# Performance work log

Hardware: AMD Instinct MI355X
Metric: run time of the kernel (lower is better)

## Reference

```python
import jax, jax.numpy as jnp
import numpy as np

B = 32768
MAXD = 60               # max raw feature dim (user)
DIMS = [60, 51, 43]     # user, event, space
H = 256                 # HIDDEN_DIM
E = 256                 # EMBED_DIM
NH = 4                  # num heads
HD = H // NH            # head dim = 64
SCALE = float(np.sqrt(HD))
EPS = 1e-5


def setup_inputs() -> dict:
    key = jax.random.key(0)
    ks = iter(jax.random.split(key, 64))
    def rn(shape, scale=0.05):
        return jax.random.normal(next(ks), shape, dtype=jnp.float32) * scale
    inp = {}
    inp["anchor_feats"] = jax.random.normal(next(ks), (B, MAXD), dtype=jnp.float32)
    inp["item_feats"] = jax.random.normal(next(ks), (B, MAXD), dtype=jnp.float32)
    inp["anchor_type_ids"] = jax.random.randint(next(ks), (B,), 0, 3, dtype=jnp.int32)
    inp["item_type_ids"] = jax.random.randint(next(ks), (B,), 0, 3, dtype=jnp.int32)
    # per-type encoder MLPs; W1 zero-padded beyond each type's input dim (matches torch slicing x[:, :dim])
    W1 = rn((3, MAXD, H))
    row_mask = np.zeros((3, MAXD, 1), dtype=np.float32)
    for t, d in enumerate(DIMS):
        row_mask[t, :d, 0] = 1.0
    inp["enc_W1"] = W1 * jnp.asarray(row_mask)
    inp["enc_b1"] = rn((3, H)); inp["enc_g1"] = jnp.ones((3, H)); inp["enc_be1"] = jnp.zeros((3, H))
    inp["enc_W2"] = rn((3, H, H))
    inp["enc_b2"] = rn((3, H)); inp["enc_g2"] = jnp.ones((3, H)); inp["enc_be2"] = jnp.zeros((3, H))
    # two stacked HGT layers; 9 edge types (src*3+dst), 3 node types
    inp["hgt_Wk"] = rn((2, 9, H, H)); inp["hgt_Wq"] = rn((2, 9, H, H)); inp["hgt_Wv"] = rn((2, 9, H, H))
    inp["hgt_Wout"] = rn((2, 3, H, H))
    inp["hgt_g"] = jnp.ones((2, 3, H)); inp["hgt_b"] = jnp.zeros((2, 3, H))
    inp["out_W"] = rn((H, E)); inp["out_b"] = rn((E,))
    inp["out_g"] = jnp.ones((E,)); inp["out_be"] = jnp.zeros((E,))
    return inp


def _ln(x, g, b):
    m = x.mean(-1, keepdims=True)
    v = ((x - m) ** 2).mean(-1, keepdims=True)
    return (x - m) / jnp.sqrt(v + EPS) * g + b


def _encode(feats, tids, W1, b1, g1, be1, W2, b2, g2, be2):
    # per-type 2-layer MLP (Linear->LN->ReLU x2, dropout=eval noop), masked select
    h = jnp.zeros((feats.shape[0], H), feats.dtype)
    for t in range(3):
        z = jax.nn.relu(_ln(feats @ W1[t] + b1[t], g1[t], be1[t]))
        z = jax.nn.relu(_ln(z @ W2[t] + b2[t], g2[t], be2[t]))
        h = jnp.where((tids == t)[:, None], z, h)
    return h


def _hgt_apply(Wk, Wq, Wv, Wout, g, b, e, dt, src_h, dst_h):
    # single-dim dot-product attention per head, sigmoid gate
    Bn = src_h.shape[0]
    k = (src_h @ Wk[e]).reshape(Bn, NH, HD)
    q = (dst_h @ Wq[e]).reshape(Bn, NH, HD)
    v = (src_h @ Wv[e]).reshape(Bn, NH, HD)
    attn = jax.nn.sigmoid((q * k).sum(-1, keepdims=True) / SCALE)
    msg = (attn * v).reshape(Bn, H)
    return _ln(dst_h + msg @ Wout[dt], g[dt], b[dt])


def _hgt_hop(Wk, Wq, Wv, Wout, g, b, ha, hi, atid, itid):
    # torch code: ha_out from clone of ha, hi updated per disjoint (atype,itype) mask,
    # both updates read ORIGINAL ha/hi for each masked element
    ha_new, hi_new = ha, hi
    for a in range(3):
        for i in range(3):
            mask = ((atid == a) & (itid == i))[:, None]
            ua = _hgt_apply(Wk, Wq, Wv, Wout, g, b, i * 3 + a, a, hi, ha)  # item -> anchor
            ui = _hgt_apply(Wk, Wq, Wv, Wout, g, b, a * 3 + i, i, ha, hi)  # anchor -> item
            ha_new = jnp.where(mask, ua, ha_new)
            hi_new = jnp.where(mask, ui, hi_new)
    return ha_new, hi_new


def _l2norm(x):
    return x / jnp.maximum(jnp.linalg.norm(x, axis=-1, keepdims=True), 1e-12)


def reference(anchor_feats, item_feats, anchor_type_ids, item_type_ids,
              enc_W1, enc_b1, enc_g1, enc_be1, enc_W2, enc_b2, enc_g2, enc_be2,
              hgt_Wk, hgt_Wq, hgt_Wv, hgt_Wout, hgt_g, hgt_b,
              out_W, out_b, out_g, out_be):
    ha = _encode(anchor_feats, anchor_type_ids, enc_W1, enc_b1, enc_g1, enc_be1, enc_W2, enc_b2, enc_g2, enc_be2)
    hi = _encode(item_feats, item_type_ids, enc_W1, enc_b1, enc_g1, enc_be1, enc_W2, enc_b2, enc_g2, enc_be2)
    for L in range(2):
        ha, hi = _hgt_hop(hgt_Wk[L], hgt_Wq[L], hgt_Wv[L], hgt_Wout[L], hgt_g[L], hgt_b[L],
                          ha, hi, anchor_type_ids, item_type_ids)
    anchor_emb = _l2norm(_ln(ha @ out_W + out_b, out_g, out_be))
    item_emb = _l2norm(_ln(hi @ out_W + out_b, out_g, out_be))
    return anchor_emb, item_emb
```

## Files before the change

### kernel.cpp

```cpp
#include <hip/hip_runtime.h>
#include <math.h>

#define BN   32768
#define MAXD 60
#define HDIM 256
#define TR   16
#define LDX  264

typedef __attribute__((ext_vector_type(4))) float f32x4;
typedef __attribute__((ext_vector_type(8))) short bf16x8;

#define MFMA(a, b, c) __builtin_amdgcn_mfma_f32_16x16x32_bf16(a, b, c, 0, 0, 0)

__device__ __forceinline__ unsigned short f2bf(float f) {
  union { float f; unsigned u; } v; v.f = f;
  unsigned r = v.u + 0x7FFF + ((v.u >> 16) & 1);
  return (unsigned short)(r >> 16);
}

template <int LDXE>
__device__ __forceinline__ bf16x8 ldsAx(const unsigned short* buf, int rf,
                                        int ks, int lane) {
  const int row = rf * 16 + (lane & 15);
  const int ko = ks * 32 + ((lane >> 4) << 3);
  return *(const bf16x8*)(buf + row * LDXE + ko);
}

template <int KS>
__device__ __forceinline__ bf16x8 fragB(const unsigned short* __restrict__ W,
                                        int cfw, int ks, int lane) {
  return *(const bf16x8*)(W + ((size_t)(cfw * KS + ks) << 9) + (lane << 3));
}

__device__ __forceinline__ float red16(float p) {
  p += __shfl_xor(p, 1); p += __shfl_xor(p, 2);
  p += __shfl_xor(p, 4); p += __shfl_xor(p, 8);
  return p;
}

__device__ __forceinline__ void cross_ln(float* redS, float* redQ,
                                         const float sums[2][4],
                                         const float sumq[2][4], int lane,
                                         int wid, float mo[2][4],
                                         float ro[2][4]) {
  __syncthreads();
  if ((lane & 15) == 0) {
    #pragma unroll
    for (int rf = 0; rf < 2; ++rf)
      #pragma unroll
      for (int rr = 0; rr < 4; ++rr) {
        const int row = rf * 16 + ((lane >> 4) << 2) + rr;
        redS[row * 4 + wid] = sums[rf][rr];
        redQ[row * 4 + wid] = sumq[rf][rr];
      }
  }
  __syncthreads();
  #pragma unroll
  for (int rf = 0; rf < 2; ++rf)
    #pragma unroll
    for (int rr = 0; rr < 4; ++rr) {
      const int row = rf * 16 + ((lane >> 4) << 2) + rr;
      float s = redS[row * 4] + redS[row * 4 + 1] + redS[row * 4 + 2] + redS[row * 4 + 3];
      float z = redQ[row * 4] + redQ[row * 4 + 1] + redQ[row * 4 + 2] + redQ[row * 4 + 3];
      float m = s * (1.0f / HDIM);
      mo[rf][rr] = m;
      ro[rf][rr] = rsqrtf(z * (1.0f / HDIM) - m * m + 1e-5f);
    }
}


__device__ __forceinline__ void row_reduce(float* red, const float acc[TR],
                                           float m[TR], float rs[TR], int j) {
  const int lane = j & 63, wv = j >> 6;
  __syncthreads();
  #pragma unroll
  for (int r = 0; r < TR; ++r) {
    float s = acc[r], q = acc[r] * acc[r];
    #pragma unroll
    for (int o = 32; o; o >>= 1) { s += __shfl_xor(s, o); q += __shfl_xor(q, o); }
    if (lane == 0) { red[r * 8 + wv * 2] = s; red[r * 8 + wv * 2 + 1] = q; }
  }
  __syncthreads();
  #pragma unroll
  for (int r = 0; r < TR; ++r) {
    float s = red[r * 8 + 0] + red[r * 8 + 2] + red[r * 8 + 4] + red[r * 8 + 6];
    float q = red[r * 8 + 1] + red[r * 8 + 3] + red[r * 8 + 5] + red[r * 8 + 7];
    float mean = s * (1.0f / HDIM);
    float var  = q * (1.0f / HDIM) - mean * mean;
    m[r]  = mean;
    rs[r] = rsqrtf(var + 1e-5f);
  }
}

template <int KD, int ST>
__device__ __forceinline__ void matvec_l(const float* __restrict__ W,
                                         const float* zz, float acc[TR], int j) {
  #pragma unroll 2
  for (int k = 0; k < KD; k += 4) {
    const float w0 = W[(k + 0) * HDIM + j];
    const float w1 = W[(k + 1) * HDIM + j];
    const float w2 = W[(k + 2) * HDIM + j];
    const float w3 = W[(k + 3) * HDIM + j];
    #pragma unroll
    for (int r = 0; r < TR; ++r) {
      const float4 x = *(const float4*)(zz + r * ST + k);
      acc[r] = fmaf(x.w, w3, fmaf(x.z, w2, fmaf(x.y, w1, fmaf(x.x, w0, acc[r]))));
    }
  }
}


__global__ __launch_bounds__(256) void bucket_kernel(
    const int* __restrict__ atid, const int* __restrict__ itid,
    int* cnts, int* idxA, int* idxI, int* idxC) {
  __shared__ int lcnt[15], lbase[15];
  const int tid = threadIdx.x;
  const int r = blockIdx.x * 256 + tid;
  if (tid < 15) lcnt[tid] = 0;
  __syncthreads();
  const int a = atid[r], i = itid[r];
  const int c = a * 3 + i;
  const int la = atomicAdd(&lcnt[a], 1);
  const int li = atomicAdd(&lcnt[3 + i], 1);
  const int lc = atomicAdd(&lcnt[6 + c], 1);
  __syncthreads();
  if (tid < 15) lbase[tid] = atomicAdd(&cnts[tid], lcnt[tid]);
  __syncthreads();
  idxA[a * BN + lbase[a] + la] = r;
  idxI[i * BN + lbase[3 + i] + li] = r;
  idxC[c * BN + lbase[6 + c] + lc] = r;
}


__global__ __launch_bounds__(256) void wpack_kernel(
    const float* __restrict__ src, unsigned short* __restrict__ dst,
    int nmat, int KS, int srcK) {
  const int per = KS * 8192;
  const int idx = blockIdx.x * 256 + threadIdx.x;
  const int m = idx / per;
  if (m >= nmat) return;
  const int r = idx % per;
  const int e = r & 7;
  const int lane = (r >> 3) & 63;
  const int t = r >> 9;
  const int ks = t % KS;
  const int cfw = t / KS;
  const int n = ((cfw >> 2) << 6) + ((cfw & 3) << 4) + (lane & 15);
  const int k = (ks << 5) + ((lane >> 4) << 3) + e;
  const float v = (k < srcK) ? src[(size_t)m * srcK * 256 + (size_t)k * 256 + n] : 0.0f;
  dst[idx] = f2bf(v);
}


struct EncSmem {
  unsigned short x1[32 * 72];
  unsigned short z[32 * LDX];
  float redS[32 * 4];
  float redQ[32 * 4];
  int rowsL[32];
};

__global__ __launch_bounds__(256) void enc_mfma_kernel(
    const float* __restrict__ af, const float* __restrict__ itf,
    const int* __restrict__ idxA, const int* __restrict__ idxI,
    const int* __restrict__ cnts,
    const unsigned short* __restrict__ pW1, const unsigned short* __restrict__ pW2,
    const float* __restrict__ b1, const float* __restrict__ g1,
    const float* __restrict__ be1, const float* __restrict__ b2,
    const float* __restrict__ g2, const float* __restrict__ be2,
    float* __restrict__ ha, float* __restrict__ hi) {
  const int t = blockIdx.y, ent = blockIdx.z;
  const int cnt = cnts[ent * 3 + t];
  const int base = blockIdx.x * 32;
  if (base >= cnt) return;
  const float* feats = ent ? itf : af;
  const int* idx = (ent ? idxI : idxA) + t * BN;
  float* hout = ent ? hi : ha;
  __shared__ EncSmem sm;
  const int tid = threadIdx.x, lane = tid & 63, wid = tid >> 6;

  if (tid < 32) {
    int rr = base + tid; if (rr > cnt - 1) rr = cnt - 1;
    sm.rowsL[tid] = idx[rr];
  }
  __syncthreads();
  {
    const int c2 = (tid & 31) * 2, rh = tid >> 5;
    #pragma unroll
    for (int p = 0; p < 4; ++p) {
      const int r = p * 8 + rh;
      unsigned val = 0;
      if (c2 < MAXD) {
        const float2 v = *(const float2*)(feats + (size_t)sm.rowsL[r] * MAXD + c2);
        val = (unsigned)f2bf(v.x) | ((unsigned)f2bf(v.y) << 16);
      }
      *(unsigned*)(sm.x1 + r * 72 + c2) = val;
    }
  }
  int mg[8];
  #pragma unroll
  for (int rf = 0; rf < 2; ++rf)
    #pragma unroll
    for (int rr = 0; rr < 4; ++rr)
      mg[rf * 4 + rr] = sm.rowsL[rf * 16 + ((lane >> 4) << 2) + rr];
  __syncthreads();

  f32x4 acc[2][4] = {};
  #pragma unroll
  for (int ks = 0; ks < 2; ++ks) {
    bf16x8 a0 = ldsAx<72>(sm.x1, 0, ks, lane);
    bf16x8 a1 = ldsAx<72>(sm.x1, 1, ks, lane);
    #pragma unroll
    for (int cf = 0; cf < 4; ++cf) {
      bf16x8 w = fragB<2>(pW1 + (size_t)t * 16384, (wid << 2) + cf, ks, lane);
      acc[0][cf] = MFMA(a0, w, acc[0][cf]);
      acc[1][cf] = MFMA(a1, w, acc[1][cf]);
    }
  }
  float cb[4], cg[4], cbe[4];
  #pragma unroll
  for (int cf = 0; cf < 4; ++cf) {
    const int col = (wid << 6) + (cf << 4) + (lane & 15);
    cb[cf] = b1[t * HDIM + col]; cg[cf] = g1[t * HDIM + col]; cbe[cf] = be1[t * HDIM + col];
  }
  float sums[2][4] = {}, sumq[2][4] = {};
  #pragma unroll
  for (int rf = 0; rf < 2; ++rf)
    #pragma unroll
    for (int cf = 0; cf < 4; ++cf)
      #pragma unroll
      for (int rr = 0; rr < 4; ++rr) {
        float x = acc[rf][cf][rr] + cb[cf];
        acc[rf][cf][rr] = x;
        sums[rf][rr] += x; sumq[rf][rr] += x * x;
      }
  #pragma unroll
  for (int rf = 0; rf < 2; ++rf)
    #pragma unroll
    for (int rr = 0; rr < 4; ++rr) { sums[rf][rr] = red16(sums[rf][rr]); sumq[rf][rr] = red16(sumq[rf][rr]); }
  float m[2][4], rs[2][4];
  cross_ln(sm.redS, sm.redQ, sums, sumq, lane, wid, m, rs);
  #pragma unroll
  for (int rf = 0; rf < 2; ++rf)
    #pragma unroll
    for (int cf = 0; cf < 4; ++cf) {
      const int col = (wid << 6) + (cf << 4) + (lane & 15);
      #pragma unroll
      for (int rr = 0; rr < 4; ++rr) {
        const int row = rf * 16 + ((lane >> 4) << 2) + rr;
        float zz = fmaxf((acc[rf][cf][rr] - m[rf][rr]) * rs[rf][rr] * cg[cf] + cbe[cf], 0.0f);
        sm.z[row * LDX + col] = f2bf(zz);
      }
    }
  __syncthreads();

  #pragma unroll
  for (int rf = 0; rf < 2; ++rf)
    #pragma unroll
    for (int cf = 0; cf < 4; ++cf) acc[rf][cf] = (f32x4){0.f, 0.f, 0.f, 0.f};
  #pragma unroll 2
  for (int ks = 0; ks < 8; ++ks) {
    bf16x8 a0 = ldsAx<LDX>(sm.z, 0, ks, lane);
    bf16x8 a1 = ldsAx<LDX>(sm.z, 1, ks, lane);
    #pragma unroll
    for (int cf = 0; cf < 4; ++cf) {
      bf16x8 w = fragB<8>(pW2 + (size_t)t * 65536, (wid << 2) + cf, ks, lane);
      acc[0][cf] = MFMA(a0, w, acc[0][cf]);
      acc[1][cf] = MFMA(a1, w, acc[1][cf]);
    }
  }
  #pragma unroll
  for (int cf = 0; cf < 4; ++cf) {
    const int col = (wid << 6) + (cf << 4) + (lane & 15);
    cb[cf] = b2[t * HDIM + col]; cg[cf] = g2[t * HDIM + col]; cbe[cf] = be2[t * HDIM + col];
  }
  float sums2[2][4] = {}, sumq2[2][4] = {};
  #pragma unroll
  for (int rf = 0; rf < 2; ++rf)
    #pragma unroll
    for (int cf = 0; cf < 4; ++cf)
      #pragma unroll
      for (int rr = 0; rr < 4; ++rr) {
        float x = acc[rf][cf][rr] + cb[cf];
        acc[rf][cf][rr] = x;
        sums2[rf][rr] += x; sumq2[rf][rr] += x * x;
      }
  #pragma unroll
  for (int rf = 0; rf < 2; ++rf)
    #pragma unroll
    for (int rr = 0; rr < 4; ++rr) { sums2[rf][rr] = red16(sums2[rf][rr]); sumq2[rf][rr] = red16(sumq2[rf][rr]); }
  cross_ln(sm.redS, sm.redQ, sums2, sumq2, lane, wid, m, rs);
  #pragma unroll
  for (int rf = 0; rf < 2; ++rf)
    #pragma unroll
    for (int cf = 0; cf < 4; ++cf) {
      const int col = (wid << 6) + (cf << 4) + (lane & 15);
      #pragma unroll
      for (int rr = 0; rr < 4; ++rr)
        hout[(size_t)mg[rf * 4 + rr] * HDIM + col] =
            fmaxf((acc[rf][cf][rr] - m[rf][rr]) * rs[rf][rr] * cg[cf] + cbe[cf], 0.0f);
    }
}


struct HopSmem {
  unsigned short xa[32 * LDX];
  unsigned short xi[32 * LDX];
  unsigned short msg[32 * LDX];
  float redS[32 * 4];
  float redQ[32 * 4];
  int rowsL[32];
};

__device__ __forceinline__ void hop_dir(
    const unsigned short* __restrict__ bq, const unsigned short* __restrict__ bk,
    const unsigned short* __restrict__ bv, const unsigned short* __restrict__ bo,
    const float* __restrict__ gg, const float* __restrict__ bb,
    const unsigned short* xdst, const unsigned short* xsrc,
    const float* __restrict__ hdst_g, float* __restrict__ hout_g,
    HopSmem& sm, const int mg[8], int lane, int wid) {
  f32x4 q[2][4] = {}; f32x4 kk[2][4] = {};
  #pragma unroll 2
  for (int ks = 0; ks < 8; ++ks) {
    bf16x8 ad0 = ldsAx<LDX>(xdst, 0, ks, lane), ad1 = ldsAx<LDX>(xdst, 1, ks, lane);
    bf16x8 as0 = ldsAx<LDX>(xsrc, 0, ks, lane), as1 = ldsAx<LDX>(xsrc, 1, ks, lane);
    #pragma unroll
    for (int cf = 0; cf < 4; ++cf) {
      bf16x8 wq = fragB<8>(bq, (wid << 2) + cf, ks, lane);
      bf16x8 wk = fragB<8>(bk, (wid << 2) + cf, ks, lane);
      q[0][cf]  = MFMA(ad0, wq, q[0][cf]);
      q[1][cf]  = MFMA(ad1, wq, q[1][cf]);
      kk[0][cf] = MFMA(as0, wk, kk[0][cf]);
      kk[1][cf] = MFMA(as1, wk, kk[1][cf]);
    }
  }
  float at[2][4];
  #pragma unroll
  for (int rf = 0; rf < 2; ++rf)
    #pragma unroll
    for (int rr = 0; rr < 4; ++rr) {
      float p = q[rf][0][rr] * kk[rf][0][rr] + q[rf][1][rr] * kk[rf][1][rr]
              + q[rf][2][rr] * kk[rf][2][rr] + q[rf][3][rr] * kk[rf][3][rr];
      p = red16(p);
      at[rf][rr] = 1.0f / (1.0f + __expf(-p * 0.125f));
    }
  f32x4 vv[2][4] = {};
  #pragma unroll 2
  for (int ks = 0; ks < 8; ++ks) {
    bf16x8 as0 = ldsAx<LDX>(xsrc, 0, ks, lane), as1 = ldsAx<LDX>(xsrc, 1, ks, lane);
    #pragma unroll
    for (int cf = 0; cf < 4; ++cf) {
      bf16x8 wv = fragB<8>(bv, (wid << 2) + cf, ks, lane);
      vv[0][cf] = MFMA(as0, wv, vv[0][cf]);
      vv[1][cf] = MFMA(as1, wv, vv[1][cf]);
    }
  }
  __syncthreads();
  #pragma unroll
  for (int rf = 0; rf < 2; ++rf)
    #pragma unroll
    for (int cf = 0; cf < 4; ++cf) {
      const int col = (wid << 6) + (cf << 4) + (lane & 15);
      #pragma unroll
      for (int rr = 0; rr < 4; ++rr) {
        const int row = rf * 16 + ((lane >> 4) << 2) + rr;
        sm.msg[row * LDX + col] = f2bf(vv[rf][cf][rr] * at[rf][rr]);
      }
    }
  __syncthreads();
  f32x4 oo[2][4] = {};
  #pragma unroll 2
  for (int ks = 0; ks < 8; ++ks) {
    bf16x8 am0 = ldsAx<LDX>(sm.msg, 0, ks, lane), am1 = ldsAx<LDX>(sm.msg, 1, ks, lane);
    #pragma unroll
    for (int cf = 0; cf < 4; ++cf) {
      bf16x8 wo = fragB<8>(bo, (wid << 2) + cf, ks, lane);
      oo[0][cf] = MFMA(am0, wo, oo[0][cf]);
      oo[1][cf] = MFMA(am1, wo, oo[1][cf]);
    }
  }
  float sums[2][4] = {}, sumq[2][4] = {};
  #pragma unroll
  for (int rf = 0; rf < 2; ++rf)
    #pragma unroll
    for (int cf = 0; cf < 4; ++cf) {
      const int col = (wid << 6) + (cf << 4) + (lane & 15);
      #pragma unroll
      for (int rr = 0; rr < 4; ++rr) {
        float x = hdst_g[(size_t)mg[rf * 4 + rr] * HDIM + col] + oo[rf][cf][rr];
        oo[rf][cf][rr] = x;
        sums[rf][rr] += x;
        sumq[rf][rr] += x * x;
      }
    }
  #pragma unroll
  for (int rf = 0; rf < 2; ++rf)
    #pragma unroll
    for (int rr = 0; rr < 4; ++rr) { sums[rf][rr] = red16(sums[rf][rr]); sumq[rf][rr] = red16(sumq[rf][rr]); }
  float m[2][4], rs[2][4];
  cross_ln(sm.redS, sm.redQ, sums, sumq, lane, wid, m, rs);
  float g4[4], b4[4];
  #pragma unroll
  for (int cf = 0; cf < 4; ++cf) {
    const int col = (wid << 6) + (cf << 4) + (lane & 15);
    g4[cf] = gg[col]; b4[cf] = bb[col];
  }
  #pragma unroll
  for (int rf = 0; rf < 2; ++rf)
    #pragma unroll
    for (int rr = 0; rr < 4; ++rr) {
      #pragma unroll
      for (int cf = 0; cf < 4; ++cf) {
        const int col = (wid << 6) + (cf << 4) + (lane & 15);
        hout_g[(size_t)mg[rf * 4 + rr] * HDIM + col] =
            (oo[rf][cf][rr] - m[rf][rr]) * rs[rf][rr] * g4[cf] + b4[cf];
      }
    }
}

__global__ __launch_bounds__(256) void hop_mfma_kernel(
    const unsigned short* __restrict__ bWk, const unsigned short* __restrict__ bWq,
    const unsigned short* __restrict__ bWv, const unsigned short* __restrict__ bWo,
    const float* __restrict__ g, const float* __restrict__ b,
    const int* __restrict__ idxC, const int* __restrict__ cnts,
    float* __restrict__ ha, float* __restrict__ hi) {
  const int c = blockIdx.y, a = c / 3, i = c % 3;
  const int cnt = cnts[6 + c];
  const int base = blockIdx.x * 32;
  if (base >= cnt) return;
  __shared__ HopSmem sm;
  const int tid = threadIdx.x;
  const int lane = tid & 63, wid = tid >> 6;

  if (tid < 32) {
    int rr = base + tid; if (rr > cnt - 1) rr = cnt - 1;
    sm.rowsL[tid] = idxC[c * BN + rr];
  }
  __syncthreads();
  const int cp = (tid & 127) * 2, rh = tid >> 7;
  #pragma unroll 4
  for (int r0 = 0; r0 < 32; r0 += 2) {
    const int r = r0 + rh;
    const size_t gb = (size_t)sm.rowsL[r] * HDIM + cp;
    float2 va = *(const float2*)(ha + gb);
    float2 vi = *(const float2*)(hi + gb);
    *(unsigned*)(sm.xa + r * LDX + cp) =
        (unsigned)f2bf(va.x) | ((unsigned)f2bf(va.y) << 16);
    *(unsigned*)(sm.xi + r * LDX + cp) =
        (unsigned)f2bf(vi.x) | ((unsigned)f2bf(vi.y) << 16);
  }
  int mg[8];
  #pragma unroll
  for (int rf = 0; rf < 2; ++rf)
    #pragma unroll
    for (int rr = 0; rr < 4; ++rr)
      mg[rf * 4 + rr] = sm.rowsL[rf * 16 + ((lane >> 4) << 2) + rr];
  __syncthreads();

  const size_t MS = (size_t)HDIM * HDIM;
  const int e1 = i * 3 + a;
  const int e2 = a * 3 + i;
  hop_dir(bWq + e1 * MS, bWk + e1 * MS, bWv + e1 * MS, bWo + a * MS,
          g + a * HDIM, b + a * HDIM, sm.xa, sm.xi, ha, ha, sm, mg, lane, wid);
  hop_dir(bWq + e2 * MS, bWk + e2 * MS, bWv + e2 * MS, bWo + i * MS,
          g + i * HDIM, b + i * HDIM, sm.xi, sm.xa, hi, hi, sm, mg, lane, wid);
}


struct OutSmem {
  unsigned short x[32 * LDX];
  float redS[32 * 4];
  float redQ[32 * 4];
};

__global__ __launch_bounds__(256) void out_mfma_kernel(
    const unsigned short* __restrict__ pW, const float* __restrict__ bb,
    const float* __restrict__ g, const float* __restrict__ be,
    float* __restrict__ out) {
  const int ent = blockIdx.y;
  const int base = blockIdx.x * 32;
  float* hsrc = out + (size_t)ent * BN * HDIM;
  __shared__ OutSmem sm;
  const int tid = threadIdx.x, lane = tid & 63, wid = tid >> 6;
  const int cp = (tid & 127) * 2, rh = tid >> 7;
  #pragma unroll 4
  for (int r0 = 0; r0 < 32; r0 += 2) {
    const int r = r0 + rh;
    const float2 v = *(const float2*)(hsrc + (size_t)(base + r) * HDIM + cp);
    *(unsigned*)(sm.x + r * LDX + cp) =
        (unsigned)f2bf(v.x) | ((unsigned)f2bf(v.y) << 16);
  }
  __syncthreads();
  f32x4 acc[2][4] = {};
  #pragma unroll 2
  for (int ks = 0; ks < 8; ++ks) {
    bf16x8 a0 = ldsAx<LDX>(sm.x, 0, ks, lane);
    bf16x8 a1 = ldsAx<LDX>(sm.x, 1, ks, lane);
    #pragma unroll
    for (int cf = 0; cf < 4; ++cf) {
      bf16x8 w = fragB<8>(pW, (wid << 2) + cf, ks, lane);
      acc[0][cf] = MFMA(a0, w, acc[0][cf]);
      acc[1][cf] = MFMA(a1, w, acc[1][cf]);
    }
  }
  float cb[4], cg[4], cbe[4];
  #pragma unroll
  for (int cf = 0; cf < 4; ++cf) {
    const int col = (wid << 6) + (cf << 4) + (lane & 15);
    cb[cf] = bb[col]; cg[cf] = g[col]; cbe[cf] = be[col];
  }
  float sums[2][4] = {}, sumq[2][4] = {};
  #pragma unroll
  for (int rf = 0; rf < 2; ++rf)
    #pragma unroll
    for (int cf = 0; cf < 4; ++cf)
      #pragma unroll
      for (int rr = 0; rr < 4; ++rr) {
        float x = acc[rf][cf][rr] + cb[cf];
        acc[rf][cf][rr] = x;
        sums[rf][rr] += x; sumq[rf][rr] += x * x;
      }
  #pragma unroll
  for (int rf = 0; rf < 2; ++rf)
    #pragma unroll
    for (int rr = 0; rr < 4; ++rr) { sums[rf][rr] = red16(sums[rf][rr]); sumq[rf][rr] = red16(sumq[rf][rr]); }
  float m[2][4], rs[2][4];
  cross_ln(sm.redS, sm.redQ, sums, sumq, lane, wid, m, rs);
  float s2[2][4] = {};
  #pragma unroll
  for (int rf = 0; rf < 2; ++rf)
    #pragma unroll
    for (int cf = 0; cf < 4; ++cf)
      #pragma unroll
      for (int rr = 0; rr < 4; ++rr) {
        float y = (acc[rf][cf][rr] - m[rf][rr]) * rs[rf][rr] * cg[cf] + cbe[cf];
        acc[rf][cf][rr] = y;
        s2[rf][rr] += y * y;
      }
  #pragma unroll
  for (int rf = 0; rf < 2; ++rf)
    #pragma unroll
    for (int rr = 0; rr < 4; ++rr) s2[rf][rr] = red16(s2[rf][rr]);
  __syncthreads();
  if ((lane & 15) == 0) {
    #pragma unroll
    for (int rf = 0; rf < 2; ++rf)
      #pragma unroll
      for (int rr = 0; rr < 4; ++rr) {
        const int row = rf * 16 + ((lane >> 4) << 2) + rr;
        sm.redS[row * 4 + wid] = s2[rf][rr];
      }
  }
  __syncthreads();
  #pragma unroll
  for (int rf = 0; rf < 2; ++rf)
    #pragma unroll
    for (int rr = 0; rr < 4; ++rr) {
      const int row = rf * 16 + ((lane >> 4) << 2) + rr;
      float ss = sm.redS[row * 4] + sm.redS[row * 4 + 1] +
                 sm.redS[row * 4 + 2] + sm.redS[row * 4 + 3];
      float inv = 1.0f / fmaxf(sqrtf(ss), 1e-12f);
      #pragma unroll
      for (int cf = 0; cf < 4; ++cf) {
        const int col = (wid << 6) + (cf << 4) + (lane & 15);
        hsrc[(size_t)(base + row) * HDIM + col] = acc[rf][cf][rr] * inv;
      }
    }
}


__global__ __launch_bounds__(256) void enc_kernel(
    const float* __restrict__ af, const float* __restrict__ itf,
    const int* __restrict__ idxA, const int* __restrict__ idxI,
    const int* __restrict__ cnts,
    const float* __restrict__ W1, const float* __restrict__ b1,
    const float* __restrict__ g1, const float* __restrict__ be1,
    const float* __restrict__ W2, const float* __restrict__ b2,
    const float* __restrict__ g2, const float* __restrict__ be2,
    float* __restrict__ ha, float* __restrict__ hi) {
  const int t = blockIdx.y, ent = blockIdx.z;
  const int cnt = cnts[ent * 3 + t];
  const int base = blockIdx.x * TR;
  if (base >= cnt) return;
  const int nr = (cnt - base < TR) ? (cnt - base) : TR;
  const int j = threadIdx.x;
  const float* feats = ent ? itf : af;
  const int* idx = (ent ? idxI : idxA) + t * BN;
  float* hout = ent ? hi : ha;
  __shared__ __align__(16) float xl[TR * 64];
  __shared__ __align__(16) float z[TR * HDIM];
  __shared__ float red[TR * 8];
  int rows[TR];
  #pragma unroll
  for (int r = 0; r < TR; ++r) {
    int rr = base + r; if (rr > cnt - 1) rr = cnt - 1;
    rows[r] = idx[rr];
  }
  if (j < 64) {
    #pragma unroll
    for (int r = 0; r < TR; ++r)
      xl[r * 64 + j] = (j < MAXD) ? feats[(size_t)rows[r] * MAXD + j] : 0.0f;
  }
  __syncthreads();
  float acc[TR];
  const float bj = b1[t * HDIM + j];
  #pragma unroll
  for (int r = 0; r < TR; ++r) acc[r] = bj;
  matvec_l<MAXD, 64>(W1 + (size_t)t * MAXD * HDIM, xl, acc, j);
  float m[TR], rs[TR];
  row_reduce(red, acc, m, rs, j);
  const float g1j = g1[t * HDIM + j], be1j = be1[t * HDIM + j];
  #pragma unroll
  for (int r = 0; r < TR; ++r)
    z[r * HDIM + j] = fmaxf((acc[r] - m[r]) * rs[r] * g1j + be1j, 0.0f);
  __syncthreads();
  const float b2j = b2[t * HDIM + j];
  #pragma unroll
  for (int r = 0; r < TR; ++r) acc[r] = b2j;
  matvec_l<HDIM, HDIM>(W2 + (size_t)t * HDIM * HDIM, z, acc, j);
  row_reduce(red, acc, m, rs, j);
  const float g2j = g2[t * HDIM + j], be2j = be2[t * HDIM + j];
  #pragma unroll
  for (int r = 0; r < TR; ++r)
    if (r < nr)
      hout[(size_t)rows[r] * HDIM + j] =
          fmaxf((acc[r] - m[r]) * rs[r] * g2j + be2j, 0.0f);
}

__device__ __forceinline__ void hgt_dir_f32(
    const float* __restrict__ Wq, const float* __restrict__ Wk,
    const float* __restrict__ Wv, const float* __restrict__ Wo,
    const float* __restrict__ gg, const float* __restrict__ bb,
    const float* dstl, const float* srcl, float* msg, float* red, int j,
    float res[TR]) {
  float q[TR], kk[TR];
  #pragma unroll
  for (int r = 0; r < TR; ++r) { q[r] = 0.0f; kk[r] = 0.0f; }
  matvec_l<HDIM, HDIM>(Wq, dstl, q, j);
  matvec_l<HDIM, HDIM>(Wk, srcl, kk, j);
  float attn[TR];
  #pragma unroll
  for (int r = 0; r < TR; ++r) {
    float p = q[r] * kk[r];
    #pragma unroll
    for (int o = 32; o; o >>= 1) p += __shfl_xor(p, o);
    attn[r] = 1.0f / (1.0f + expf(-p * 0.125f));
  }
  #pragma unroll
  for (int r = 0; r < TR; ++r) q[r] = 0.0f;
  matvec_l<HDIM, HDIM>(Wv, srcl, q, j);
  __syncthreads();
  #pragma unroll
  for (int r = 0; r < TR; ++r) msg[r * HDIM + j] = attn[r] * q[r];
  __syncthreads();
  float o[TR];
  #pragma unroll
  for (int r = 0; r < TR; ++r) o[r] = 0.0f;
  matvec_l<HDIM, HDIM>(Wo, msg, o, j);
  float u[TR], m[TR], rs[TR];
  #pragma unroll
  for (int r = 0; r < TR; ++r) u[r] = dstl[r * HDIM + j] + o[r];
  row_reduce(red, u, m, rs, j);
  const float gj = gg[j], bj = bb[j];
  #pragma unroll
  for (int r = 0; r < TR; ++r) res[r] = (u[r] - m[r]) * rs[r] * gj + bj;
}

__global__ __launch_bounds__(256) void hop_kernel(
    const float* __restrict__ Wk, const float* __restrict__ Wq,
    const float* __restrict__ Wv, const float* __restrict__ Wout,
    const float* __restrict__ g, const float* __restrict__ b,
    const int* __restrict__ idxC, const int* __restrict__ cnts,
    float* __restrict__ ha, float* __restrict__ hi) {
  const int c = blockIdx.y, a = c / 3, i = c % 3;
  const int cnt = cnts[6 + c];
  const int base = blockIdx.x * TR;
  if (base >= cnt) return;
  const int nr = (cnt - base < TR) ? (cnt - base) : TR;
  const int j = threadIdx.x;
  __shared__ __align__(16) float xa[TR * HDIM];
  __shared__ __align__(16) float xi[TR * HDIM];
  __shared__ __align__(16) float msg[TR * HDIM];
  __shared__ float red[TR * 8];
  int rows[TR];
  #pragma unroll
  for (int r = 0; r < TR; ++r) {
    int rr = base + r; if (rr > cnt - 1) rr = cnt - 1;
    rows[r] = idxC[c * BN + rr];
  }
  #pragma unroll
  for (int r = 0; r < TR; ++r) {
    xa[r * HDIM + j] = ha[(size_t)rows[r] * HDIM + j];
    xi[r * HDIM + j] = hi[(size_t)rows[r] * HDIM + j];
  }
  __syncthreads();
  const int e1 = i * 3 + a, e2 = a * 3 + i;
  float res1[TR], res2[TR];
  hgt_dir_f32(Wq + (size_t)e1 * HDIM * HDIM, Wk + (size_t)e1 * HDIM * HDIM,
              Wv + (size_t)e1 * HDIM * HDIM, Wout + (size_t)a * HDIM * HDIM,
              g + a * HDIM, b + a * HDIM, xa, xi, msg, red, j, res1);
  hgt_dir_f32(Wq + (size_t)e2 * HDIM * HDIM, Wk + (size_t)e2 * HDIM * HDIM,
              Wv + (size_t)e2 * HDIM * HDIM, Wout + (size_t)i * HDIM * HDIM,
              g + i * HDIM, b + i * HDIM, xi, xa, msg, red, j, res2);
  #pragma unroll
  for (int r = 0; r < TR; ++r)
    if (r < nr) {
      ha[(size_t)rows[r] * HDIM + j] = res1[r];
      hi[(size_t)rows[r] * HDIM + j] = res2[r];
    }
}

__global__ __launch_bounds__(256) void out_kernel(
    const float* __restrict__ W, const float* __restrict__ bb,
    const float* __restrict__ g, const float* __restrict__ be,
    float* __restrict__ out) {
  const int ent = blockIdx.y;
  const int base = blockIdx.x * TR;
  const int j = threadIdx.x;
  float* hsrc = out + (size_t)ent * BN * HDIM;
  __shared__ __align__(16) float xl[TR * HDIM];
  __shared__ float red[TR * 8];
  #pragma unroll
  for (int r = 0; r < TR; ++r)
    xl[r * HDIM + j] = hsrc[(size_t)(base + r) * HDIM + j];
  __syncthreads();
  float acc[TR];
  const float bj = bb[j];
  #pragma unroll
  for (int r = 0; r < TR; ++r) acc[r] = bj;
  matvec_l<HDIM, HDIM>(W, xl, acc, j);
  float m[TR], rs[TR];
  row_reduce(red, acc, m, rs, j);
  const float gj = g[j], bej = be[j];
  float y[TR];
  #pragma unroll
  for (int r = 0; r < TR; ++r) y[r] = (acc[r] - m[r]) * rs[r] * gj + bej;
  const int lane = j & 63, wv = j >> 6;
  __syncthreads();
  #pragma unroll
  for (int r = 0; r < TR; ++r) {
    float p = y[r] * y[r];
    #pragma unroll
    for (int o = 32; o; o >>= 1) p += __shfl_xor(p, o);
    if (lane == 0) red[r * 4 + wv] = p;
  }
  __syncthreads();
  #pragma unroll
  for (int r = 0; r < TR; ++r) {
    float ss = red[r * 4] + red[r * 4 + 1] + red[r * 4 + 2] + red[r * 4 + 3];
    float inv = 1.0f / fmaxf(sqrtf(ss), 1e-12f);
    hsrc[(size_t)(base + r) * HDIM + j] = y[r] * inv;
  }
}


extern "C" void kernel_launch(void* const* d_in, const int* in_sizes, int n_in,
                              void* d_out, int out_size, void* d_ws,
                              size_t ws_size, hipStream_t stream) {
  const float* af   = (const float*)d_in[0];
  const float* itf  = (const float*)d_in[1];
  const int*   atid = (const int*)d_in[2];
  const int*   itid = (const int*)d_in[3];
  const float* eW1  = (const float*)d_in[4];
  const float* eb1  = (const float*)d_in[5];
  const float* eg1  = (const float*)d_in[6];
  const float* ebe1 = (const float*)d_in[7];
  const float* eW2  = (const float*)d_in[8];
  const float* eb2  = (const float*)d_in[9];
  const float* eg2  = (const float*)d_in[10];
  const float* ebe2 = (const float*)d_in[11];
  const float* hWk  = (const float*)d_in[12];
  const float* hWq  = (const float*)d_in[13];
  const float* hWv  = (const float*)d_in[14];
  const float* hWo  = (const float*)d_in[15];
  const float* hg   = (const float*)d_in[16];
  const float* hb   = (const float*)d_in[17];
  const float* oW   = (const float*)d_in[18];
  const float* ob   = (const float*)d_in[19];
  const float* og   = (const float*)d_in[20];
  const float* obe  = (const float*)d_in[21];

  float* out = (float*)d_out;
  float* ha = out;
  float* hi = out + (size_t)BN * HDIM;

  int* cnts = (int*)d_ws;
  int* idxA = cnts + 16;
  int* idxI = idxA + 3 * BN;
  int* idxC = idxI + 3 * BN;
  unsigned short* pW1 = (unsigned short*)(idxC + 9 * BN);
  unsigned short* pW2 = pW1 + 3 * 16384;
  unsigned short* pWk = pW2 + 3 * 65536;
  unsigned short* pWq = pWk + 18 * 65536;
  unsigned short* pWv = pWq + 18 * 65536;
  unsigned short* pWo = pWv + 18 * 65536;
  unsigned short* pOW = pWo + 6 * 65536;
  const size_t ws_need = (size_t)(16 + 15 * BN) * 4 +
                         ((size_t)3 * 16384 + (size_t)64 * 65536) * 2;
  const bool use_mfma = ws_size >= ws_need;

  hipMemsetAsync(cnts, 0, 16 * sizeof(int), stream);
  bucket_kernel<<<BN / 256, 256, 0, stream>>>(atid, itid, cnts, idxA, idxI, idxC);

  if (use_mfma) {
    wpack_kernel<<<3 * 16384 / 256, 256, 0, stream>>>(eW1, pW1, 3, 2, 60);
    wpack_kernel<<<3 * 65536 / 256, 256, 0, stream>>>(eW2, pW2, 3, 8, 256);
    wpack_kernel<<<18 * 65536 / 256, 256, 0, stream>>>(hWk, pWk, 18, 8, 256);
    wpack_kernel<<<18 * 65536 / 256, 256, 0, stream>>>(hWq, pWq, 18, 8, 256);
    wpack_kernel<<<18 * 65536 / 256, 256, 0, stream>>>(hWv, pWv, 18, 8, 256);
    wpack_kernel<<<6 * 65536 / 256, 256, 0, stream>>>(hWo, pWo, 6, 8, 256);
    wpack_kernel<<<65536 / 256, 256, 0, stream>>>(oW, pOW, 1, 8, 256);

    enc_mfma_kernel<<<dim3(BN / 32, 3, 2), 256, 0, stream>>>(
        af, itf, idxA, idxI, cnts, pW1, pW2,
        eb1, eg1, ebe1, eb2, eg2, ebe2, ha, hi);
    for (int L = 0; L < 2; ++L) {
      hop_mfma_kernel<<<dim3(BN / 32, 9), 256, 0, stream>>>(
          pWk + (size_t)L * 9 * 65536, pWq + (size_t)L * 9 * 65536,
          pWv + (size_t)L * 9 * 65536, pWo + (size_t)L * 3 * 65536,
          hg + L * 3 * HDIM, hb + L * 3 * HDIM, idxC, cnts, ha, hi);
    }
    out_mfma_kernel<<<dim3(BN / 32, 2), 256, 0, stream>>>(pOW, ob, og, obe, out);
  } else {
    enc_kernel<<<dim3((BN + TR - 1) / TR, 3, 2), 256, 0, stream>>>(
        af, itf, idxA, idxI, cnts, eW1, eb1, eg1, ebe1, eW2, eb2, eg2, ebe2,
        ha, hi);
    for (int L = 0; L < 2; ++L) {
      hop_kernel<<<dim3((BN + TR - 1) / TR, 9), 256, 0, stream>>>(
          hWk + (size_t)L * 9 * HDIM * HDIM, hWq + (size_t)L * 9 * HDIM * HDIM,
          hWv + (size_t)L * 9 * HDIM * HDIM, hWo + (size_t)L * 3 * HDIM * HDIM,
          hg + L * 3 * HDIM, hb + L * 3 * HDIM, idxC, cnts, ha, hi);
    }
    out_kernel<<<dim3(BN / TR, 2), 256, 0, stream>>>(oW, ob, og, obe, out);
  }
}
```

Before: 324.2 us.

## Fuse encoder, both HGT hops and output projection into one per-pair kernel

Replaces the separate encoder, two hop, and output kernels with one fused kernel. Each block handles 32 rows of one (anchor type, item type) pair and keeps the anchor and item hidden states in registers and LDS across all stages. This removes the fp32 global round trips of ha/hi between stages and several kernel launches. In exchange, the encoder work is grouped by pair bucket and blocks carry more register state. The LDS row stride also changes from 264 to 260.

```diff
diff --git a/kernel.cpp b/kernel.cpp
--- a/kernel.cpp
+++ b/kernel.cpp
@@ -5,7 +5,7 @@
 #define MAXD 60
 #define HDIM 256
 #define TR   16
-#define LDX  264
+#define LDX  260
 
 typedef __attribute__((ext_vector_type(4))) float f32x4;
 typedef __attribute__((ext_vector_type(8))) short bf16x8;
@@ -37,6 +37,15 @@
   p += __shfl_xor(p, 4); p += __shfl_xor(p, 8);
   return p;
 }
+
+struct FSmem {
+  unsigned short xa[32 * LDX];
+  unsigned short xi[32 * LDX];
+  unsigned short msg[32 * LDX];
+  float redS[128];
+  float redQ[128];
+  int rowsL[32];
+};
 
 __device__ __forceinline__ void cross_ln(float* redS, float* redQ,
                                          const float sums[2][4],
@@ -66,47 +75,6 @@
       mo[rf][rr] = m;
       ro[rf][rr] = rsqrtf(z * (1.0f / HDIM) - m * m + 1e-5f);
     }
-}
-
-
-__device__ __forceinline__ void row_reduce(float* red, const float acc[TR],
-                                           float m[TR], float rs[TR], int j) {
-  const int lane = j & 63, wv = j >> 6;
-  __syncthreads();
-  #pragma unroll
-  for (int r = 0; r < TR; ++r) {
-    float s = acc[r], q = acc[r] * acc[r];
-    #pragma unroll
-    for (int o = 32; o; o >>= 1) { s += __shfl_xor(s, o); q += __shfl_xor(q, o); }
-    if (lane == 0) { red[r * 8 + wv * 2] = s; red[r * 8 + wv * 2 + 1] = q; }
-  }
-  __syncthreads();
-  #pragma unroll
-  for (int r = 0; r < TR; ++r) {
-    float s = red[r * 8 + 0] + red[r * 8 + 2] + red[r * 8 + 4] + red[r * 8 + 6];
-    float q = red[r * 8 + 1] + red[r * 8 + 3] + red[r * 8 + 5] + red[r * 8 + 7];
-    float mean = s * (1.0f / HDIM);
-    float var  = q * (1.0f / HDIM) - mean * mean;
-    m[r]  = mean;
-    rs[r] = rsqrtf(var + 1e-5f);
-  }
-}
-
-template <int KD, int ST>
-__device__ __forceinline__ void matvec_l(const float* __restrict__ W,
-                                         const float* zz, float acc[TR], int j) {
-  #pragma unroll 2
-  for (int k = 0; k < KD; k += 4) {
-    const float w0 = W[(k + 0) * HDIM + j];
-    const float w1 = W[(k + 1) * HDIM + j];
-    const float w2 = W[(k + 2) * HDIM + j];
-    const float w3 = W[(k + 3) * HDIM + j];
-    #pragma unroll
-    for (int r = 0; r < TR; ++r) {
-      const float4 x = *(const float4*)(zz + r * ST + k);
-      acc[r] = fmaf(x.w, w3, fmaf(x.z, w2, fmaf(x.y, w1, fmaf(x.x, w0, acc[r]))));
-    }
-  }
 }
 
 
@@ -152,38 +120,15 @@
 }
 
 
-struct EncSmem {
-  unsigned short x1[32 * 72];
-  unsigned short z[32 * LDX];
-  float redS[32 * 4];
-  float redQ[32 * 4];
-  int rowsL[32];
-};
-
-__global__ __launch_bounds__(256) void enc_mfma_kernel(
-    const float* __restrict__ af, const float* __restrict__ itf,
-    const int* __restrict__ idxA, const int* __restrict__ idxI,
-    const int* __restrict__ cnts,
+__device__ __forceinline__ void enc_pass(
+    const float* __restrict__ feats, int t,
     const unsigned short* __restrict__ pW1, const unsigned short* __restrict__ pW2,
     const float* __restrict__ b1, const float* __restrict__ g1,
     const float* __restrict__ be1, const float* __restrict__ b2,
     const float* __restrict__ g2, const float* __restrict__ be2,
-    float* __restrict__ ha, float* __restrict__ hi) {
-  const int t = blockIdx.y, ent = blockIdx.z;
-  const int cnt = cnts[ent * 3 + t];
-  const int base = blockIdx.x * 32;
-  if (base >= cnt) return;
-  const float* feats = ent ? itf : af;
-  const int* idx = (ent ? idxI : idxA) + t * BN;
-  float* hout = ent ? hi : ha;
-  __shared__ EncSmem sm;
-  const int tid = threadIdx.x, lane = tid & 63, wid = tid >> 6;
-
-  if (tid < 32) {
-    int rr = base + tid; if (rr > cnt - 1) rr = cnt - 1;
-    sm.rowsL[tid] = idx[rr];
-  }
-  __syncthreads();
+    FSmem& sm, unsigned short* xbuf, f32x4 resF[2][4],
+    int tid, int lane, int wid) {
+  unsigned short* x1 = sm.msg;
   {
     const int c2 = (tid & 31) * 2, rh = tid >> 5;
     #pragma unroll
@@ -194,22 +139,16 @@
         const float2 v = *(const float2*)(feats + (size_t)sm.rowsL[r] * MAXD + c2);
         val = (unsigned)f2bf(v.x) | ((unsigned)f2bf(v.y) << 16);
       }
-      *(unsigned*)(sm.x1 + r * 72 + c2) = val;
-    }
-  }
-  int mg[8];
-  #pragma unroll
-  for (int rf = 0; rf < 2; ++rf)
-    #pragma unroll
-    for (int rr = 0; rr < 4; ++rr)
-      mg[rf * 4 + rr] = sm.rowsL[rf * 16 + ((lane >> 4) << 2) + rr];
+      *(unsigned*)(x1 + r * 72 + c2) = val;
+    }
+  }
   __syncthreads();
 
   f32x4 acc[2][4] = {};
   #pragma unroll
   for (int ks = 0; ks < 2; ++ks) {
-    bf16x8 a0 = ldsAx<72>(sm.x1, 0, ks, lane);
-    bf16x8 a1 = ldsAx<72>(sm.x1, 1, ks, lane);
+    bf16x8 a0 = ldsAx<72>(x1, 0, ks, lane);
+    bf16x8 a1 = ldsAx<72>(x1, 1, ks, lane);
     #pragma unroll
     for (int cf = 0; cf < 4; ++cf) {
       bf16x8 w = fragB<2>(pW1 + (size_t)t * 16384, (wid << 2) + cf, ks, lane);
@@ -249,7 +188,7 @@
       for (int rr = 0; rr < 4; ++rr) {
         const int row = rf * 16 + ((lane >> 4) << 2) + rr;
         float zz = fmaxf((acc[rf][cf][rr] - m[rf][rr]) * rs[rf][rr] * cg[cf] + cbe[cf], 0.0f);
-        sm.z[row * LDX + col] = f2bf(zz);
+        xbuf[row * LDX + col] = f2bf(zz);
       }
     }
   __syncthreads();
@@ -260,8 +199,8 @@
     for (int cf = 0; cf < 4; ++cf) acc[rf][cf] = (f32x4){0.f, 0.f, 0.f, 0.f};
   #pragma unroll 2
   for (int ks = 0; ks < 8; ++ks) {
-    bf16x8 a0 = ldsAx<LDX>(sm.z, 0, ks, lane);
-    bf16x8 a1 = ldsAx<LDX>(sm.z, 1, ks, lane);
+    bf16x8 a0 = ldsAx<LDX>(xbuf, 0, ks, lane);
+    bf16x8 a1 = ldsAx<LDX>(xbuf, 1, ks, lane);
     #pragma unroll
     for (int cf = 0; cf < 4; ++cf) {
       bf16x8 w = fragB<8>(pW2 + (size_t)t * 65536, (wid << 2) + cf, ks, lane);
@@ -296,29 +235,22 @@
     for (int cf = 0; cf < 4; ++cf) {
       const int col = (wid << 6) + (cf << 4) + (lane & 15);
       #pragma unroll
-      for (int rr = 0; rr < 4; ++rr)
-        hout[(size_t)mg[rf * 4 + rr] * HDIM + col] =
-            fmaxf((acc[rf][cf][rr] - m[rf][rr]) * rs[rf][rr] * cg[cf] + cbe[cf], 0.0f);
-    }
-}
-
-
-struct HopSmem {
-  unsigned short xa[32 * LDX];
-  unsigned short xi[32 * LDX];
-  unsigned short msg[32 * LDX];
-  float redS[32 * 4];
-  float redQ[32 * 4];
-  int rowsL[32];
-};
+      for (int rr = 0; rr < 4; ++rr) {
+        float v = fmaxf((acc[rf][cf][rr] - m[rf][rr]) * rs[rf][rr] * cg[cf] + cbe[cf], 0.0f);
+        resF[rf][cf][rr] = v;
+        const int row = rf * 16 + ((lane >> 4) << 2) + rr;
+        xbuf[row * LDX + col] = f2bf(v);
+      }
+    }
+  __syncthreads();
+}
 
 __device__ __forceinline__ void hop_dir(
     const unsigned short* __restrict__ bq, const unsigned short* __restrict__ bk,
     const unsigned short* __restrict__ bv, const unsigned short* __restrict__ bo,
     const float* __restrict__ gg, const float* __restrict__ bb,
     const unsigned short* xdst, const unsigned short* xsrc,
-    const float* __restrict__ hdst_g, float* __restrict__ hout_g,
-    HopSmem& sm, const int mg[8], int lane, int wid) {
+    FSmem& sm, f32x4 resF[2][4], int lane, int wid) {
   f32x4 q[2][4] = {}; f32x4 kk[2][4] = {};
   #pragma unroll 2
   for (int ks = 0; ks < 8; ++ks) {
@@ -383,16 +315,14 @@
   #pragma unroll
   for (int rf = 0; rf < 2; ++rf)
     #pragma unroll
-    for (int cf = 0; cf < 4; ++cf) {
-      const int col = (wid << 6) + (cf << 4) + (lane & 15);
-      #pragma unroll
-      for (int rr = 0; rr < 4; ++rr) {
-        float x = hdst_g[(size_t)mg[rf * 4 + rr] * HDIM + col] + oo[rf][cf][rr];
+    for (int cf = 0; cf < 4; ++cf)
+      #pragma unroll
+      for (int rr = 0; rr < 4; ++rr) {
+        float x = resF[rf][cf][rr] + oo[rf][cf][rr];
         oo[rf][cf][rr] = x;
         sums[rf][rr] += x;
         sumq[rf][rr] += x * x;
       }
-    }
   #pragma unroll
   for (int rf = 0; rf < 2; ++rf)
     #pragma unroll
@@ -408,94 +338,22 @@
   #pragma unroll
   for (int rf = 0; rf < 2; ++rf)
     #pragma unroll
-    for (int rr = 0; rr < 4; ++rr) {
-      #pragma unroll
-      for (int cf = 0; cf < 4; ++cf) {
-        const int col = (wid << 6) + (cf << 4) + (lane & 15);
-        hout_g[(size_t)mg[rf * 4 + rr] * HDIM + col] =
-            (oo[rf][cf][rr] - m[rf][rr]) * rs[rf][rr] * g4[cf] + b4[cf];
-      }
-    }
-}
-
-__global__ __launch_bounds__(256) void hop_mfma_kernel(
-    const unsigned short* __restrict__ bWk, const unsigned short* __restrict__ bWq,
-    const unsigned short* __restrict__ bWv, const unsigned short* __restrict__ bWo,
-    const float* __restrict__ g, const float* __restrict__ b,
-    const int* __restrict__ idxC, const int* __restrict__ cnts,
-    float* __restrict__ ha, float* __restrict__ hi) {
-  const int c = blockIdx.y, a = c / 3, i = c % 3;
-  const int cnt = cnts[6 + c];
-  const int base = blockIdx.x * 32;
-  if (base >= cnt) return;
-  __shared__ HopSmem sm;
-  const int tid = threadIdx.x;
-  const int lane = tid & 63, wid = tid >> 6;
-
-  if (tid < 32) {
-    int rr = base + tid; if (rr > cnt - 1) rr = cnt - 1;
-    sm.rowsL[tid] = idxC[c * BN + rr];
-  }
-  __syncthreads();
-  const int cp = (tid & 127) * 2, rh = tid >> 7;
-  #pragma unroll 4
-  for (int r0 = 0; r0 < 32; r0 += 2) {
-    const int r = r0 + rh;
-    const size_t gb = (size_t)sm.rowsL[r] * HDIM + cp;
-    float2 va = *(const float2*)(ha + gb);
-    float2 vi = *(const float2*)(hi + gb);
-    *(unsigned*)(sm.xa + r * LDX + cp) =
-        (unsigned)f2bf(va.x) | ((unsigned)f2bf(va.y) << 16);
-    *(unsigned*)(sm.xi + r * LDX + cp) =
-        (unsigned)f2bf(vi.x) | ((unsigned)f2bf(vi.y) << 16);
-  }
-  int mg[8];
-  #pragma unroll
-  for (int rf = 0; rf < 2; ++rf)
-    #pragma unroll
-    for (int rr = 0; rr < 4; ++rr)
-      mg[rf * 4 + rr] = sm.rowsL[rf * 16 + ((lane >> 4) << 2) + rr];
-  __syncthreads();
-
-  const size_t MS = (size_t)HDIM * HDIM;
-  const int e1 = i * 3 + a;
-  const int e2 = a * 3 + i;
-  hop_dir(bWq + e1 * MS, bWk + e1 * MS, bWv + e1 * MS, bWo + a * MS,
-          g + a * HDIM, b + a * HDIM, sm.xa, sm.xi, ha, ha, sm, mg, lane, wid);
-  hop_dir(bWq + e2 * MS, bWk + e2 * MS, bWv + e2 * MS, bWo + i * MS,
-          g + i * HDIM, b + i * HDIM, sm.xi, sm.xa, hi, hi, sm, mg, lane, wid);
-}
-
-
-struct OutSmem {
-  unsigned short x[32 * LDX];
-  float redS[32 * 4];
-  float redQ[32 * 4];
-};
-
-__global__ __launch_bounds__(256) void out_mfma_kernel(
-    const unsigned short* __restrict__ pW, const float* __restrict__ bb,
-    const float* __restrict__ g, const float* __restrict__ be,
-    float* __restrict__ out) {
-  const int ent = blockIdx.y;
-  const int base = blockIdx.x * 32;
-  float* hsrc = out + (size_t)ent * BN * HDIM;
-  __shared__ OutSmem sm;
-  const int tid = threadIdx.x, lane = tid & 63, wid = tid >> 6;
-  const int cp = (tid & 127) * 2, rh = tid >> 7;
-  #pragma unroll 4
-  for (int r0 = 0; r0 < 32; r0 += 2) {
-    const int r = r0 + rh;
-    const float2 v = *(const float2*)(hsrc + (size_t)(base + r) * HDIM + cp);
-    *(unsigned*)(sm.x + r * LDX + cp) =
-        (unsigned)f2bf(v.x) | ((unsigned)f2bf(v.y) << 16);
-  }
-  __syncthreads();
+    for (int cf = 0; cf < 4; ++cf)
+      #pragma unroll
+      for (int rr = 0; rr < 4; ++rr)
+        resF[rf][cf][rr] = (oo[rf][cf][rr] - m[rf][rr]) * rs[rf][rr] * g4[cf] + b4[cf];
+}
+
+__device__ __forceinline__ void out_pass(
+    const unsigned short* xbuf, const unsigned short* __restrict__ pW,
+    const float* __restrict__ bb, const float* __restrict__ gg,
+    const float* __restrict__ be, FSmem& sm, const int mg[8],
+    float* __restrict__ hout, int lane, int wid) {
   f32x4 acc[2][4] = {};
   #pragma unroll 2
   for (int ks = 0; ks < 8; ++ks) {
-    bf16x8 a0 = ldsAx<LDX>(sm.x, 0, ks, lane);
-    bf16x8 a1 = ldsAx<LDX>(sm.x, 1, ks, lane);
+    bf16x8 a0 = ldsAx<LDX>(xbuf, 0, ks, lane);
+    bf16x8 a1 = ldsAx<LDX>(xbuf, 1, ks, lane);
     #pragma unroll
     for (int cf = 0; cf < 4; ++cf) {
       bf16x8 w = fragB<8>(pW, (wid << 2) + cf, ks, lane);
@@ -507,7 +365,7 @@
   #pragma unroll
   for (int cf = 0; cf < 4; ++cf) {
     const int col = (wid << 6) + (cf << 4) + (lane & 15);
-    cb[cf] = bb[col]; cg[cf] = g[col]; cbe[cf] = be[col];
+    cb[cf] = bb[col]; cg[cf] = gg[col]; cbe[cf] = be[col];
   }
   float sums[2][4] = {}, sumq[2][4] = {};
   #pragma unroll
@@ -563,11 +421,131 @@
       #pragma unroll
       for (int cf = 0; cf < 4; ++cf) {
         const int col = (wid << 6) + (cf << 4) + (lane & 15);
-        hsrc[(size_t)(base + row) * HDIM + col] = acc[rf][cf][rr] * inv;
-      }
-    }
-}
-
+        hout[(size_t)mg[rf * 4 + rr] * HDIM + col] = acc[rf][cf][rr] * inv;
+      }
+    }
+  __syncthreads();
+}
+
+
+__global__ __launch_bounds__(256) void fused_kernel(
+    const float* __restrict__ af, const float* __restrict__ itf,
+    const int* __restrict__ idxC, const int* __restrict__ cnts,
+    const unsigned short* __restrict__ pW1, const unsigned short* __restrict__ pW2,
+    const float* __restrict__ eb1, const float* __restrict__ eg1,
+    const float* __restrict__ ebe1, const float* __restrict__ eb2,
+    const float* __restrict__ eg2, const float* __restrict__ ebe2,
+    const unsigned short* __restrict__ pWk, const unsigned short* __restrict__ pWq,
+    const unsigned short* __restrict__ pWv, const unsigned short* __restrict__ pWo,
+    const float* __restrict__ hg, const float* __restrict__ hb,
+    const unsigned short* __restrict__ pOW, const float* __restrict__ ob,
+    const float* __restrict__ og, const float* __restrict__ obe,
+    float* __restrict__ out) {
+  const int l = blockIdx.x;
+  int c, rb;
+  if (l < 8192) { c = l & 7; rb = l >> 3; }
+  else          { c = 8;     rb = l - 8192; }
+  const int cnt = cnts[6 + c];
+  const int base = rb * 32;
+  if (base >= cnt) return;
+  const int a = c / 3, i = c % 3;
+
+  __shared__ FSmem sm;
+  const int tid = threadIdx.x, lane = tid & 63, wid = tid >> 6;
+
+  if (tid < 32) {
+    int rr = base + tid; if (rr > cnt - 1) rr = cnt - 1;
+    sm.rowsL[tid] = idxC[c * BN + rr];
+  }
+  __syncthreads();
+  int mg[8];
+  #pragma unroll
+  for (int rf = 0; rf < 2; ++rf)
+    #pragma unroll
+    for (int rr = 0; rr < 4; ++rr)
+      mg[rf * 4 + rr] = sm.rowsL[rf * 16 + ((lane >> 4) << 2) + rr];
+
+  f32x4 haF[2][4], hiF[2][4];
+  enc_pass(af, a, pW1, pW2, eb1, eg1, ebe1, eb2, eg2, ebe2,
+           sm, sm.xa, haF, tid, lane, wid);
+  enc_pass(itf, i, pW1, pW2, eb1, eg1, ebe1, eb2, eg2, ebe2,
+           sm, sm.xi, hiF, tid, lane, wid);
+
+  const size_t MS = (size_t)HDIM * HDIM;
+  const int e1 = i * 3 + a;
+  const int e2 = a * 3 + i;
+  #pragma unroll 1
+  for (int L = 0; L < 2; ++L) {
+    const unsigned short* Wk = pWk + (size_t)L * 9 * MS;
+    const unsigned short* Wq = pWq + (size_t)L * 9 * MS;
+    const unsigned short* Wv = pWv + (size_t)L * 9 * MS;
+    const unsigned short* Wo = pWo + (size_t)L * 3 * MS;
+    const float* g = hg + L * 3 * HDIM;
+    const float* b = hb + L * 3 * HDIM;
+    hop_dir(Wq + e1 * MS, Wk + e1 * MS, Wv + e1 * MS, Wo + a * MS,
+            g + a * HDIM, b + a * HDIM, sm.xa, sm.xi, sm, haF, lane, wid);
+    hop_dir(Wq + e2 * MS, Wk + e2 * MS, Wv + e2 * MS, Wo + i * MS,
+            g + i * HDIM, b + i * HDIM, sm.xi, sm.xa, sm, hiF, lane, wid);
+    __syncthreads();
+    #pragma unroll
+    for (int rf = 0; rf < 2; ++rf)
+      #pragma unroll
+      for (int cf = 0; cf < 4; ++cf) {
+        const int col = (wid << 6) + (cf << 4) + (lane & 15);
+        #pragma unroll
+        for (int rr = 0; rr < 4; ++rr) {
+          const int row = rf * 16 + ((lane >> 4) << 2) + rr;
+          sm.xa[row * LDX + col] = f2bf(haF[rf][cf][rr]);
+          sm.xi[row * LDX + col] = f2bf(hiF[rf][cf][rr]);
+        }
+      }
+    __syncthreads();
+  }
+
+  out_pass(sm.xa, pOW, ob, og, obe, sm, mg, out, lane, wid);
+  out_pass(sm.xi, pOW, ob, og, obe, sm, mg, out + (size_t)BN * HDIM, lane, wid);
+}
+
+
+__device__ __forceinline__ void row_reduce(float* red, const float acc[TR],
+                                           float m[TR], float rs[TR], int j) {
+  const int lane = j & 63, wv = j >> 6;
+  __syncthreads();
+  #pragma unroll
+  for (int r = 0; r < TR; ++r) {
+    float s = acc[r], q = acc[r] * acc[r];
+    #pragma unroll
+    for (int o = 32; o; o >>= 1) { s += __shfl_xor(s, o); q += __shfl_xor(q, o); }
+    if (lane == 0) { red[r * 8 + wv * 2] = s; red[r * 8 + wv * 2 + 1] = q; }
+  }
+  __syncthreads();
+  #pragma unroll
+  for (int r = 0; r < TR; ++r) {
+    float s = red[r * 8 + 0] + red[r * 8 + 2] + red[r * 8 + 4] + red[r * 8 + 6];
+    float q = red[r * 8 + 1] + red[r * 8 + 3] + red[r * 8 + 5] + red[r * 8 + 7];
+    float mean = s * (1.0f / HDIM);
+    float var  = q * (1.0f / HDIM) - mean * mean;
+    m[r]  = mean;
+    rs[r] = rsqrtf(var + 1e-5f);
+  }
+}
+
+template <int KD, int ST>
+__device__ __forceinline__ void matvec_l(const float* __restrict__ W,
+                                         const float* zz, float acc[TR], int j) {
+  #pragma unroll 2
+  for (int k = 0; k < KD; k += 4) {
+    const float w0 = W[(k + 0) * HDIM + j];
+    const float w1 = W[(k + 1) * HDIM + j];
+    const float w2 = W[(k + 2) * HDIM + j];
+    const float w3 = W[(k + 3) * HDIM + j];
+    #pragma unroll
+    for (int r = 0; r < TR; ++r) {
+      const float4 x = *(const float4*)(zz + r * ST + k);
+      acc[r] = fmaf(x.w, w3, fmaf(x.z, w2, fmaf(x.y, w1, fmaf(x.x, w0, acc[r]))));
+    }
+  }
+}
 
 __global__ __launch_bounds__(256) void enc_kernel(
     const float* __restrict__ af, const float* __restrict__ itf,
@@ -781,8 +759,6 @@
   const float* obe  = (const float*)d_in[21];
 
   float* out = (float*)d_out;
-  float* ha = out;
-  float* hi = out + (size_t)BN * HDIM;
 
   int* cnts = (int*)d_ws;
   int* idxA = cnts + 16;
@@ -811,17 +787,12 @@
     wpack_kernel<<<6 * 65536 / 256, 256, 0, stream>>>(hWo, pWo, 6, 8, 256);
     wpack_kernel<<<65536 / 256, 256, 0, stream>>>(oW, pOW, 1, 8, 256);
 
-    enc_mfma_kernel<<<dim3(BN / 32, 3, 2), 256, 0, stream>>>(
-        af, itf, idxA, idxI, cnts, pW1, pW2,
-        eb1, eg1, ebe1, eb2, eg2, ebe2, ha, hi);
-    for (int L = 0; L < 2; ++L) {
-      hop_mfma_kernel<<<dim3(BN / 32, 9), 256, 0, stream>>>(
-          pWk + (size_t)L * 9 * 65536, pWq + (size_t)L * 9 * 65536,
-          pWv + (size_t)L * 9 * 65536, pWo + (size_t)L * 3 * 65536,
-          hg + L * 3 * HDIM, hb + L * 3 * HDIM, idxC, cnts, ha, hi);
-    }
-    out_mfma_kernel<<<dim3(BN / 32, 2), 256, 0, stream>>>(pOW, ob, og, obe, out);
+    fused_kernel<<<9216, 256, 0, stream>>>(
+        af, itf, idxC, cnts, pW1, pW2, eb1, eg1, ebe1, eb2, eg2, ebe2,
+        pWk, pWq, pWv, pWo, hg, hb, pOW, ob, og, obe, out);
   } else {
+    float* ha = out;
+    float* hi = out + (size_t)BN * HDIM;
     enc_kernel<<<dim3((BN + TR - 1) / TR, 3, 2), 256, 0, stream>>>(
         af, itf, idxA, idxI, cnts, eW1, eb1, eg1, ebe1, eW2, eb2, eg2, ebe2,
         ha, hi);
```

Result: slower. 616.9 us (+90.3%).
